# Optimization experiments

Hardware: AMD Instinct MI355X
Metric: run time of the kernel (lower is better)

## Reference

```python
import jax, jax.numpy as jnp
import numpy as np

B, D, C, M = 16384, 512, 1000, 8


def setup_inputs() -> dict:
    key = jax.random.key(0)
    k1, k2, k3, k4 = jax.random.split(key, 4)
    x = jax.random.normal(k1, (B, D), dtype=jnp.float32)
    W = jax.random.normal(k2, (M, D, C), dtype=jnp.float32) * 0.02
    b = jax.random.normal(k3, (M, C), dtype=jnp.float32) * 0.02
    coefs = jax.random.uniform(k4, (M,), dtype=jnp.float32, minval=0.5, maxval=1.5)
    return {"x": x, "W": W, "b": b, "coefs": coefs}


def reference(x, W, b, coefs):
    # Per-model logits: [M, B, C]
    logits = jnp.einsum('bd,mdc->mbc', x, W) + b[:, None, :]
    pos = jnp.argmax(logits, axis=-1)  # [M, B] predicted class per model/sample
    rows = jnp.broadcast_to(jnp.arange(x.shape[0])[None, :], pos.shape)  # [M, B]
    # Weighted vote scatter-add: ans[j, pos[m, j]] += coefs[m]
    ans = jnp.zeros((x.shape[0], W.shape[2]), dtype=jnp.float32)
    ans = ans.at[rows, pos].add(jnp.broadcast_to(coefs[:, None], pos.shape))
    return ans / W.shape[0]
```

## Files before the change

### kernel.cpp

```cpp
#include <hip/hip_runtime.h>

#define B_N 16384
#define D_K 512
#define C_N 1000
#define CP 1024
#define M_N 8
#define GAP_EPS 1e-3f

typedef __attribute__((ext_vector_type(8))) _Float16 f16x8;
typedef __attribute__((ext_vector_type(4))) float f32x4;

typedef const __attribute__((address_space(1))) unsigned int* gptr_t;
typedef __attribute__((address_space(3))) unsigned int* lptr_t;

__device__ __forceinline__ void gload16(const void* g, void* l) {
    __builtin_amdgcn_global_load_lds((gptr_t)g, (lptr_t)l, 16, 0, 0);
}

#define BAR()        asm volatile("s_barrier" ::: "memory")
#define WAIT_LGKM0() asm volatile("s_waitcnt lgkmcnt(0)" ::: "memory")
#define WAIT_VM6()   asm volatile("s_waitcnt vmcnt(6)" ::: "memory")
#define WAIT_VM0()   asm volatile("s_waitcnt vmcnt(0)" ::: "memory")

__device__ __forceinline__ unsigned short h16(float f) {
    _Float16 h = (_Float16)f;
    return *(unsigned short*)&h;
}


__global__ __launch_bounds__(256) void ve_conv(const float* __restrict__ x,
        const float* __restrict__ W, unsigned short* __restrict__ xf,
        unsigned short* __restrict__ wt, unsigned int* __restrict__ cnts) {
    const int tid = threadIdx.x;
    if (blockIdx.x < 8192) {
        int i = blockIdx.x * 256 + tid;
        if (blockIdx.x == 0 && tid < M_N) cnts[tid] = 0u;
        float4 v = reinterpret_cast<const float4*>(x)[i];
        ushort4 h;
        h.x = h16(v.x); h.y = h16(v.y); h.z = h16(v.z); h.w = h16(v.w);
        reinterpret_cast<ushort4*>(xf)[i] = h;
    } else {
        __shared__ float t[64][65];
        const int b = blockIdx.x - 8192;
        const int c0 = (b & 15) * 64, k0 = ((b >> 4) & 7) * 64, m = b >> 7;
#pragma unroll
        for (int p = 0; p < 16; ++p) {
            int idx = p * 256 + tid;
            int kk = idx >> 6, cc = idx & 63;
            int c = c0 + cc;
            t[kk][cc] = (c < C_N) ? W[((size_t)m * D_K + k0 + kk) * C_N + c] : 0.f;
        }
        __syncthreads();
#pragma unroll
        for (int p = 0; p < 4; ++p) {
            int idx = p * 256 + tid;
            int cc = idx >> 4, kq = idx & 15;
            ushort4 h;
            h.x = h16(t[kq * 4 + 0][cc]); h.y = h16(t[kq * 4 + 1][cc]);
            h.z = h16(t[kq * 4 + 2][cc]); h.w = h16(t[kq * 4 + 3][cc]);
            size_t o = ((size_t)m * CP + c0 + cc) * D_K + k0 + kq * 4;
            *reinterpret_cast<ushort4*>(wt + o) = h;
        }
    }
}


__global__ __launch_bounds__(256, 2) void ve_gemm16d(
        const unsigned short* __restrict__ Xf, const unsigned short* __restrict__ WT,
        const float* __restrict__ bias, float4* __restrict__ part) {
    __shared__ unsigned short At[12288];
    __shared__ unsigned short Bt[24576];

    const int tid = threadIdx.x;
    const int l = tid & 63, w = tid >> 6;
    const int wr = w >> 1, wc = w & 1;
    const int l15 = l & 15, kg = l >> 4;
    const int bid = blockIdx.x;
    const int mb = bid & 7, ct = (bid >> 3) & 3, rt = bid >> 5;
    const int r0 = rt * 128, c0 = ct * 256;

    const int lhi = l >> 3, llo = l & 7;
    const int s3g = llo ^ lhi;
    const int srow16 = (lhi << 1) | (s3g >> 2);
    const int kgs = (s3g & 3) * 8;

    const unsigned short* xA0 = Xf + (size_t)(r0 +      w * 16 + srow16) * D_K + kgs;
    const unsigned short* xA1 = Xf + (size_t)(r0 + 64 + w * 16 + srow16) * D_K + kgs;
    const unsigned short* xB0 = WT + (size_t)(mb * CP + c0 +       w * 16 + srow16) * D_K + kgs;
    const unsigned short* xB1 = WT + (size_t)(mb * CP + c0 +  64 + w * 16 + srow16) * D_K + kgs;
    const unsigned short* xB2 = WT + (size_t)(mb * CP + c0 + 128 + w * 16 + srow16) * D_K + kgs;
    const unsigned short* xB3 = WT + (size_t)(mb * CP + c0 + 192 + w * 16 + srow16) * D_K + kgs;

    auto stage = [&](int t, int buf) {
        unsigned short* A = At + buf * 4096;
        unsigned short* B = Bt + buf * 8192;
        gload16(xA0 + t * 32, A + tid * 8);
        gload16(xA1 + t * 32, A + 2048 + tid * 8);
        gload16(xB0 + t * 32, B + tid * 8);
        gload16(xB1 + t * 32, B + 2048 + tid * 8);
        gload16(xB2 + t * 32, B + 4096 + tid * 8);
        gload16(xB3 + t * 32, B + 6144 + tid * 8);
    };

    auto ldsoff = [&](int row, int kc) {
        return (row >> 1) * 64 + (((((row & 1) << 2) | kc) ^ ((row >> 1) & 7)) * 8);
    };
    const char* aP[4]; const char* bP[8];
#pragma unroll
    for (int i = 0; i < 4; ++i)
        aP[i] = (const char*)At + 2 * ldsoff(wr * 64 + i * 16 + l15, kg);
#pragma unroll
    for (int j = 0; j < 8; ++j)
        bP[j] = (const char*)Bt + wc * 8192 + 2 * ldsoff(j * 16 + l15, kg);

    f32x4 acc[4][8];
#pragma unroll
    for (int i = 0; i < 4; ++i)
#pragma unroll
        for (int j = 0; j < 8; ++j) acc[i][j] = (f32x4){0.f, 0.f, 0.f, 0.f};

    stage(0, 0);
    stage(1, 1);
    WAIT_VM6();
    BAR();

#pragma unroll 1
    for (int t = 0; t < 16; ++t) {
        if (t < 14) stage(t + 2, (t + 2) % 3);
        const int curA = (t % 3) * 8192;
        const int curB = (t % 3) * 16384;

        f16x8 af[4], bf[8];
#pragma unroll
        for (int i = 0; i < 4; ++i) af[i] = *reinterpret_cast<const f16x8*>(aP[i] + curA);
#pragma unroll
        for (int j = 0; j < 8; ++j) bf[j] = *reinterpret_cast<const f16x8*>(bP[j] + curB);
        __builtin_amdgcn_s_setprio(1);
#pragma unroll
        for (int i = 0; i < 4; ++i)
#pragma unroll
            for (int j = 0; j < 8; ++j)
                acc[i][j] = __builtin_amdgcn_mfma_f32_16x16x32_f16(af[i], bf[j], acc[i][j], 0, 0, 0);
        __builtin_amdgcn_s_setprio(0);

        if (t < 14)       { WAIT_VM6(); }
        else if (t == 14) { WAIT_VM0(); }
        WAIT_LGKM0();
        BAR();
    }

    float4 (*wtop)[2] = reinterpret_cast<float4(*)[2]>(At);

    float bv[8]; int cg[8];
#pragma unroll
    for (int j = 0; j < 8; ++j) {
        int c = c0 + wc * 128 + j * 16 + l15;
        cg[j] = c;
        bv[j] = (c < C_N) ? bias[mb * C_N + c] : -1e30f;
    }
#pragma unroll
    for (int i = 0; i < 4; ++i) {
#pragma unroll
        for (int reg = 0; reg < 4; ++reg) {
            float v1 = acc[i][0][reg] + bv[0]; int i1 = cg[0];
            float v2 = -1e30f;
#pragma unroll
            for (int j = 1; j < 8; ++j) {
                float v = acc[i][j][reg] + bv[j];
                float mn = fminf(v, v1);
                v2 = fmaxf(v2, mn);
                i1 = (v > v1) ? cg[j] : i1;
                v1 = fmaxf(v1, v);
            }
#pragma unroll
            for (int mask = 1; mask < 16; mask <<= 1) {
                float ov1 = __shfl_xor(v1, mask);
                int   oi1 = __shfl_xor(i1, mask);
                float ov2 = __shfl_xor(v2, mask);
                float mn = fminf(v1, ov1);
                v2 = fmaxf(fmaxf(v2, ov2), mn);
                i1 = (ov1 > v1) ? oi1 : i1;
                v1 = fmaxf(v1, ov1);
            }
            if (l15 == 0) {
                int row = wr * 64 + i * 16 + (l >> 4) * 4 + reg;
                wtop[row][wc] = make_float4(v1, __int_as_float(i1), v2, 0.f);
            }
        }
    }
    __syncthreads();
    if (tid < 128) {
        float4 a = wtop[tid][0], b = wtop[tid][1];
        float v1, v2; int i1;
        if (b.x > a.x) {
            v1 = b.x; i1 = __float_as_int(b.y);
            v2 = fmaxf(a.x, b.z);
        } else {
            v1 = a.x; i1 = __float_as_int(a.y);
            v2 = fmaxf(b.x, a.z);
        }
        part[((size_t)mb * B_N + r0 + tid) * 4 + ct] =
            make_float4(v1, __int_as_float(i1), v2, 0.f);
    }
}


__global__ __launch_bounds__(128) void ve_flag4(const float4* __restrict__ part,
        unsigned int* __restrict__ wout, unsigned int* __restrict__ rlist,
        unsigned int* __restrict__ cnts) {
    int r = blockIdx.x * 128 + threadIdx.x;
#pragma unroll
    for (int m = 0; m < M_N; ++m) {
        float4 o = part[((size_t)m * B_N + r) * 4 + 0];
        float v1 = o.x; int i1 = __float_as_int(o.y); float v2 = o.z;
#pragma unroll
        for (int t = 1; t < 4; ++t) {
            float4 q = part[((size_t)m * B_N + r) * 4 + t];
            if (q.x > v1) {
                v2 = fmaxf(v1, fmaxf(q.z, v2));
                v1 = q.x; i1 = __float_as_int(q.y);
            } else {
                v2 = fmaxf(v2, q.x);
            }
        }
        wout[m * B_N + r] = (unsigned)i1;
        if (v1 - v2 <= GAP_EPS) {
            unsigned pos = atomicAdd(&cnts[m], 1u);
            rlist[m * B_N + pos] = (unsigned)r;
        }
    }
}


__global__ __launch_bounds__(256) void ve_exact_g(
        const float* __restrict__ x, const float* __restrict__ W,
        const float* __restrict__ bias, const unsigned int* __restrict__ rlist,
        const unsigned int* __restrict__ cnts, float2* __restrict__ part2) {
    __shared__ float xs[32][65];
    __shared__ float wsm[32][128];
    __shared__ int rg[64];
    const int ct = blockIdx.x, m = blockIdx.z;
    const int tid = threadIdx.x;
    const int tx = tid & 15, ty = tid >> 4;
    const int c0 = ct * 128;
    const unsigned nm = cnts[m];

    for (unsigned rb = blockIdx.y; rb * 64 < nm; rb += gridDim.y) {
        __syncthreads();
        if (tid < 64) {
            unsigned idx = rb * 64 + tid;
            rg[tid] = (idx < nm) ? (int)rlist[m * B_N + idx] : 0;
        }
        __syncthreads();

        float acc[4][8];
#pragma unroll
        for (int i = 0; i < 4; i++)
#pragma unroll
            for (int j = 0; j < 8; j++) acc[i][j] = 0.f;

        for (int kt = 0; kt < D_K; kt += 32) {
#pragma unroll
            for (int i = 0; i < 2; i++) {
                int li = tid + i * 256;
                int row = li >> 3, kq = li & 7;
                float4 v = *reinterpret_cast<const float4*>(
                        x + (size_t)rg[row] * D_K + kt + kq * 4);
                int kk = kq * 4;
                xs[kk + 0][row] = v.x; xs[kk + 1][row] = v.y;
                xs[kk + 2][row] = v.z; xs[kk + 3][row] = v.w;
            }
#pragma unroll
            for (int i = 0; i < 4; i++) {
                int li = tid + i * 256;
                int kk = li >> 5, cq = li & 31;
                int c = c0 + cq * 4;
                const float* p = W + ((size_t)(m * D_K + kt + kk)) * C_N + c;
                float4 v;
                if (c + 3 < C_N) v = *reinterpret_cast<const float4*>(p);
                else {
                    v.x = (c + 0 < C_N) ? p[0] : 0.f; v.y = (c + 1 < C_N) ? p[1] : 0.f;
                    v.z = (c + 2 < C_N) ? p[2] : 0.f; v.w = (c + 3 < C_N) ? p[3] : 0.f;
                }
                wsm[kk][cq * 4 + 0] = v.x; wsm[kk][cq * 4 + 1] = v.y;
                wsm[kk][cq * 4 + 2] = v.z; wsm[kk][cq * 4 + 3] = v.w;
            }
            __syncthreads();
            for (int kk = 0; kk < 32; kk++) {
                float a[4], bb[8];
#pragma unroll
                for (int i = 0; i < 4; i++) a[i] = xs[kk][ty + i * 16];
#pragma unroll
                for (int j = 0; j < 8; j++) bb[j] = wsm[kk][tx + j * 16];
#pragma unroll
                for (int i = 0; i < 4; i++)
#pragma unroll
                    for (int j = 0; j < 8; j++) acc[i][j] += a[i] * bb[j];
            }
            __syncthreads();
        }

        const float NEG_INF = -__builtin_huge_valf();
        float bv[8]; int cv[8];
#pragma unroll
        for (int j = 0; j < 8; j++) {
            int c = c0 + tx + j * 16;
            cv[j] = c;
            bv[j] = (c < C_N) ? bias[m * C_N + c] : 0.f;
        }
#pragma unroll
        for (int i = 0; i < 4; i++) {
            float best = NEG_INF; int bidx = 0x7fffffff;
#pragma unroll
            for (int j = 0; j < 8; j++) {
                int c = cv[j];
                float v = (c < C_N) ? (acc[i][j] + bv[j]) : NEG_INF;
                if (v > best || (v == best && c < bidx)) { best = v; bidx = c; }
            }
#pragma unroll
            for (int mask = 1; mask < 16; mask <<= 1) {
                float ov = __shfl_xor(best, mask);
                int oi = __shfl_xor(bidx, mask);
                if (ov > best || (ov == best && oi < bidx)) { best = ov; bidx = oi; }
            }
            unsigned slot = rb * 64 + ty + i * 16;
            if (tx == 0 && slot < nm)
                part2[((size_t)m * B_N + slot) * 8 + ct] = make_float2(best, __int_as_float(bidx));
        }
    }
}

__global__ __launch_bounds__(256) void ve_merge_x(const float2* __restrict__ part2,
        const unsigned int* __restrict__ rlist, const unsigned int* __restrict__ cnts,
        unsigned int* __restrict__ wout) {
    int gid = blockIdx.x * 256 + threadIdx.x;
    int m = gid >> 14, s = gid & (B_N - 1);
    if (s < (int)cnts[m]) {
        const float NEG_INF = -__builtin_huge_valf();
        float best = NEG_INF; int bidx = 0x7fffffff;
#pragma unroll
        for (int ctt = 0; ctt < 8; ctt++) {
            float2 p = part2[((size_t)m * B_N + s) * 8 + ctt];
            int oi = __float_as_int(p.y);
            if (p.x > best || (p.x == best && oi < bidx)) { best = p.x; bidx = oi; }
        }
        wout[m * B_N + rlist[m * B_N + s]] = (unsigned)bidx;
    }
}

__global__ __launch_bounds__(256) void ve_votef(const unsigned int* __restrict__ wout,
        const float* __restrict__ coefs, float* __restrict__ out) {
    const int tid = threadIdx.x;
    const int r0 = blockIdx.x * 64;
    float4* po = reinterpret_cast<float4*>(out + (size_t)r0 * C_N);
    const float4 z = make_float4(0.f, 0.f, 0.f, 0.f);
    for (int i = tid; i < 16000; i += 256) po[i] = z;
    __syncthreads();
    if (tid < 64) {
        int r = r0 + tid;
#pragma unroll
        for (int m = 0; m < M_N; ++m)
            out[(size_t)r * C_N + wout[m * B_N + r]] += coefs[m] * 0.125f;
    }
}


#define TM 128
#define TN 128
#define TK 32
#define CT 8

__global__ __launch_bounds__(256) void ve_zero_out(float* __restrict__ out, int n4) {
    int i = blockIdx.x * blockDim.x + threadIdx.x;
    const float4 z = make_float4(0.f, 0.f, 0.f, 0.f);
    for (; i < n4; i += gridDim.x * blockDim.x)
        reinterpret_cast<float4*>(out)[i] = z;
}

__global__ __launch_bounds__(256) void ve_gemm_argmax_fb(
        const float* __restrict__ x, const float* __restrict__ W,
        const float* __restrict__ bias, float2* __restrict__ part) {
    __shared__ float xs[TK][TM + 1];
    __shared__ float ws[TK][TN];
    const int ct = blockIdx.x, rt = blockIdx.y, m = blockIdx.z;
    const int tid = threadIdx.x;
    const int tx = tid & 15, ty = tid >> 4;
    const int r0 = rt * TM, c0 = ct * TN;
    float acc[8][8];
#pragma unroll
    for (int i = 0; i < 8; i++)
#pragma unroll
        for (int j = 0; j < 8; j++) acc[i][j] = 0.f;
    const float* xbase = x + (size_t)r0 * D_K;
    for (int kt = 0; kt < D_K; kt += TK) {
#pragma unroll
        for (int i = 0; i < 4; i++) {
            int li = tid + i * 256;
            int row = li >> 3, kq = li & 7;
            float4 v = *reinterpret_cast<const float4*>(xbase + (size_t)row * D_K + kt + kq * 4);
            int kk = kq * 4;
            xs[kk + 0][row] = v.x; xs[kk + 1][row] = v.y;
            xs[kk + 2][row] = v.z; xs[kk + 3][row] = v.w;
        }
#pragma unroll
        for (int i = 0; i < 4; i++) {
            int li = tid + i * 256;
            int kk = li >> 5, cq = li & 31;
            int c = c0 + cq * 4;
            const float* p = W + ((size_t)(m * D_K + kt + kk)) * C_N + c;
            float4 v;
            if (c + 3 < C_N) v = *reinterpret_cast<const float4*>(p);
            else {
                v.x = (c + 0 < C_N) ? p[0] : 0.f; v.y = (c + 1 < C_N) ? p[1] : 0.f;
                v.z = (c + 2 < C_N) ? p[2] : 0.f; v.w = (c + 3 < C_N) ? p[3] : 0.f;
            }
            ws[kk][cq * 4 + 0] = v.x; ws[kk][cq * 4 + 1] = v.y;
            ws[kk][cq * 4 + 2] = v.z; ws[kk][cq * 4 + 3] = v.w;
        }
        __syncthreads();
        for (int kk = 0; kk < TK; kk++) {
            float a[8], bb[8];
#pragma unroll
            for (int i = 0; i < 8; i++) a[i] = xs[kk][ty + i * 16];
#pragma unroll
            for (int j = 0; j < 8; j++) bb[j] = ws[kk][tx + j * 16];
#pragma unroll
            for (int i = 0; i < 8; i++)
#pragma unroll
                for (int j = 0; j < 8; j++) acc[i][j] += a[i] * bb[j];
        }
        __syncthreads();
    }
    const float NEG_INF = -__builtin_huge_valf();
    float bv[8]; int cv[8];
#pragma unroll
    for (int j = 0; j < 8; j++) {
        int c = c0 + tx + j * 16;
        cv[j] = c;
        bv[j] = (c < C_N) ? bias[m * C_N + c] : 0.f;
    }
#pragma unroll
    for (int i = 0; i < 8; i++) {
        int r = r0 + ty + i * 16;
        float best = NEG_INF; int bidx = 0x7fffffff;
#pragma unroll
        for (int j = 0; j < 8; j++) {
            int c = cv[j];
            float v = (c < C_N) ? (acc[i][j] + bv[j]) : NEG_INF;
            if (v > best || (v == best && c < bidx)) { best = v; bidx = c; }
        }
#pragma unroll
        for (int mask = 1; mask < 16; mask <<= 1) {
            float ov = __shfl_xor(best, mask);
            int oi = __shfl_xor(bidx, mask);
            if (ov > best || (ov == best && oi < bidx)) { best = ov; bidx = oi; }
        }
        if (tx == 0) part[((size_t)m * B_N + r) * CT + ct] = make_float2(best, __int_as_float(bidx));
    }
}

__global__ __launch_bounds__(256) void ve_vote_fb(const float2* __restrict__ part,
        const float* __restrict__ coefs, float* __restrict__ out) {
    int r = blockIdx.x * blockDim.x + threadIdx.x;
    if (r >= B_N) return;
    const float NEG_INF = -__builtin_huge_valf();
#pragma unroll
    for (int m = 0; m < M_N; m++) {
        float best = NEG_INF; int bidx = 0x7fffffff;
#pragma unroll
        for (int ctt = 0; ctt < CT; ctt++) {
            float2 p = part[((size_t)m * B_N + r) * CT + ctt];
            int oi = __float_as_int(p.y);
            if (p.x > best || (p.x == best && oi < bidx)) { best = p.x; bidx = oi; }
        }
        out[(size_t)r * C_N + bidx] += coefs[m] * 0.125f;
    }
}


extern "C" void kernel_launch(void* const* d_in, const int* in_sizes, int n_in,
                              void* d_out, int out_size, void* d_ws, size_t ws_size,
                              hipStream_t stream) {
    const float* x     = (const float*)d_in[0];
    const float* W     = (const float*)d_in[1];
    const float* bias  = (const float*)d_in[2];
    const float* coefs = (const float*)d_in[3];
    float* out = (float*)d_out;

    const size_t NEED = (57ull << 20) + 4096;
    if (ws_size >= NEED) {
        char* ws = (char*)d_ws;
        unsigned short* Xf    = (unsigned short*)(ws);
        unsigned short* WT16  = (unsigned short*)(ws + (16ull << 20));
        float4*         part  = (float4*)(ws + (24ull << 20));
        float2*         part2 = (float2*)(ws + (40ull << 20));
        unsigned int*   wout  = (unsigned int*)(ws + (48ull << 20));
        unsigned int*   rlist = (unsigned int*)(ws + (48ull << 20) + (512ull << 10));
        unsigned int*   cnts  = (unsigned int*)(ws + (49ull << 20));

        ve_conv<<<9216, 256, 0, stream>>>(x, W, Xf, WT16, cnts);
        ve_gemm16d<<<4096, 256, 0, stream>>>(Xf, WT16, bias, part);
        ve_flag4<<<128, 128, 0, stream>>>(part, wout, rlist, cnts);
        ve_exact_g<<<dim3(8, 8, 8), 256, 0, stream>>>(x, W, bias, rlist, cnts, part2);
        ve_merge_x<<<512, 256, 0, stream>>>(part2, rlist, cnts, wout);
        ve_votef<<<256, 256, 0, stream>>>(wout, coefs, out);
    } else {
        float2* partf = (float2*)d_ws;
        ve_zero_out<<<2048, 256, 0, stream>>>(out, B_N * C_N / 4);
        dim3 grid(CT, B_N / TM, M_N);
        ve_gemm_argmax_fb<<<grid, 256, 0, stream>>>(x, W, bias, partf);
        ve_vote_fb<<<(B_N + 255) / 256, 256, 0, stream>>>(partf, coefs, out);
    }
}
```

Baseline: 314.9 us.

## Merge exact-fix results via 64-bit atomicMax and fold output zeroing into conversion

Removes the ve_merge_x kernel: ve_exact_g now writes each column-tile's best (value, index) into a per-row 64-bit key with atomicMax. The key packs an order-preserving float key with the inverted index, so ties still go to the smaller index. ve_flag4 marks ambiguous rows with a high bit in wout, and ve_votef reads the fixed key only for those rows. Zeroing the output moves into extra blocks of the conversion kernel, so votef no longer clears out before scattering. This drops one launch and the part2 buffer traffic, at the cost of global atomics and extra conversion blocks.

```diff
diff --git a/kernel.cpp b/kernel.cpp
--- a/kernel.cpp
+++ b/kernel.cpp
@@ -27,10 +27,16 @@
     return *(unsigned short*)&h;
 }
 
+__device__ __forceinline__ unsigned fkey32(float f) {
+    unsigned u = __float_as_uint(f);
+    return (u & 0x80000000u) ? ~u : (u | 0x80000000u);
+}
+
 
 __global__ __launch_bounds__(256) void ve_conv(const float* __restrict__ x,
         const float* __restrict__ W, unsigned short* __restrict__ xf,
-        unsigned short* __restrict__ wt, unsigned int* __restrict__ cnts) {
+        unsigned short* __restrict__ wt, unsigned int* __restrict__ cnts,
+        float* __restrict__ out) {
     const int tid = threadIdx.x;
     if (blockIdx.x < 8192) {
         int i = blockIdx.x * 256 + tid;
@@ -39,7 +45,7 @@
         ushort4 h;
         h.x = h16(v.x); h.y = h16(v.y); h.z = h16(v.z); h.w = h16(v.w);
         reinterpret_cast<ushort4*>(xf)[i] = h;
-    } else {
+    } else if (blockIdx.x < 9216) {
         __shared__ float t[64][65];
         const int b = blockIdx.x - 8192;
         const int c0 = (b & 15) * 64, k0 = ((b >> 4) & 7) * 64, m = b >> 7;
@@ -61,6 +67,11 @@
             size_t o = ((size_t)m * CP + c0 + cc) * D_K + k0 + kq * 4;
             *reinterpret_cast<ushort4*>(wt + o) = h;
         }
+    } else {
+        const int b = blockIdx.x - 9216;
+        float4* po = reinterpret_cast<float4*>(out) + (size_t)b * 4000;
+        const float4 z = make_float4(0.f, 0.f, 0.f, 0.f);
+        for (int i = tid; i < 4000; i += 256) po[i] = z;
     }
 }
 
@@ -207,7 +218,7 @@
 
 __global__ __launch_bounds__(128) void ve_flag4(const float4* __restrict__ part,
         unsigned int* __restrict__ wout, unsigned int* __restrict__ rlist,
-        unsigned int* __restrict__ cnts) {
+        unsigned int* __restrict__ cnts, unsigned long long* __restrict__ fixkey) {
     int r = blockIdx.x * 128 + threadIdx.x;
 #pragma unroll
     for (int m = 0; m < M_N; ++m) {
@@ -223,10 +234,13 @@
                 v2 = fmaxf(v2, q.x);
             }
         }
-        wout[m * B_N + r] = (unsigned)i1;
         if (v1 - v2 <= GAP_EPS) {
+            wout[m * B_N + r] = (unsigned)i1 | 0x80000000u;
+            fixkey[m * B_N + r] = 0ull;
             unsigned pos = atomicAdd(&cnts[m], 1u);
             rlist[m * B_N + pos] = (unsigned)r;
+        } else {
+            wout[m * B_N + r] = (unsigned)i1;
         }
     }
 }
@@ -235,7 +249,7 @@
 __global__ __launch_bounds__(256) void ve_exact_g(
         const float* __restrict__ x, const float* __restrict__ W,
         const float* __restrict__ bias, const unsigned int* __restrict__ rlist,
-        const unsigned int* __restrict__ cnts, float2* __restrict__ part2) {
+        const unsigned int* __restrict__ cnts, unsigned long long* __restrict__ fixkey) {
     __shared__ float xs[32][65];
     __shared__ float wsm[32][128];
     __shared__ int rg[64];
@@ -324,43 +338,30 @@
                 if (ov > best || (ov == best && oi < bidx)) { best = ov; bidx = oi; }
             }
             unsigned slot = rb * 64 + ty + i * 16;
-            if (tx == 0 && slot < nm)
-                part2[((size_t)m * B_N + slot) * 8 + ct] = make_float2(best, __int_as_float(bidx));
-        }
-    }
-}
-
-__global__ __launch_bounds__(256) void ve_merge_x(const float2* __restrict__ part2,
-        const unsigned int* __restrict__ rlist, const unsigned int* __restrict__ cnts,
-        unsigned int* __restrict__ wout) {
-    int gid = blockIdx.x * 256 + threadIdx.x;
-    int m = gid >> 14, s = gid & (B_N - 1);
-    if (s < (int)cnts[m]) {
-        const float NEG_INF = -__builtin_huge_valf();
-        float best = NEG_INF; int bidx = 0x7fffffff;
-#pragma unroll
-        for (int ctt = 0; ctt < 8; ctt++) {
-            float2 p = part2[((size_t)m * B_N + s) * 8 + ctt];
-            int oi = __float_as_int(p.y);
-            if (p.x > best || (p.x == best && oi < bidx)) { best = p.x; bidx = oi; }
-        }
-        wout[m * B_N + rlist[m * B_N + s]] = (unsigned)bidx;
-    }
-}
-
-__global__ __launch_bounds__(256) void ve_votef(const unsigned int* __restrict__ wout,
+            if (tx == 0 && slot < nm) {
+                unsigned long long key =
+                    ((unsigned long long)fkey32(best) << 32) | (unsigned)(~(unsigned)bidx);
+                atomicMax(fixkey + (size_t)m * B_N + rg[ty + i * 16], key);
+            }
+        }
+    }
+}
+
+__global__ __launch_bounds__(128) void ve_votef(const unsigned int* __restrict__ wout,
+        const unsigned long long* __restrict__ fixkey,
         const float* __restrict__ coefs, float* __restrict__ out) {
-    const int tid = threadIdx.x;
-    const int r0 = blockIdx.x * 64;
-    float4* po = reinterpret_cast<float4*>(out + (size_t)r0 * C_N);
-    const float4 z = make_float4(0.f, 0.f, 0.f, 0.f);
-    for (int i = tid; i < 16000; i += 256) po[i] = z;
-    __syncthreads();
-    if (tid < 64) {
-        int r = r0 + tid;
-#pragma unroll
-        for (int m = 0; m < M_N; ++m)
-            out[(size_t)r * C_N + wout[m * B_N + r]] += coefs[m] * 0.125f;
+    int r = blockIdx.x * 128 + threadIdx.x;
+#pragma unroll
+    for (int m = 0; m < M_N; ++m) {
+        unsigned wv = wout[m * B_N + r];
+        int idx;
+        if (wv & 0x80000000u) {
+            unsigned long long k = fixkey[(size_t)m * B_N + r];
+            idx = (int)(~(unsigned)k);
+        } else {
+            idx = (int)wv;
+        }
+        out[(size_t)r * C_N + idx] += coefs[m] * 0.125f;
     }
 }
 
@@ -490,20 +491,19 @@
     const size_t NEED = (57ull << 20) + 4096;
     if (ws_size >= NEED) {
         char* ws = (char*)d_ws;
-        unsigned short* Xf    = (unsigned short*)(ws);
-        unsigned short* WT16  = (unsigned short*)(ws + (16ull << 20));
-        float4*         part  = (float4*)(ws + (24ull << 20));
-        float2*         part2 = (float2*)(ws + (40ull << 20));
-        unsigned int*   wout  = (unsigned int*)(ws + (48ull << 20));
-        unsigned int*   rlist = (unsigned int*)(ws + (48ull << 20) + (512ull << 10));
-        unsigned int*   cnts  = (unsigned int*)(ws + (49ull << 20));
-
-        ve_conv<<<9216, 256, 0, stream>>>(x, W, Xf, WT16, cnts);
+        unsigned short*     Xf     = (unsigned short*)(ws);
+        unsigned short*     WT16   = (unsigned short*)(ws + (16ull << 20));
+        float4*             part   = (float4*)(ws + (24ull << 20));
+        unsigned long long* fixkey = (unsigned long long*)(ws + (40ull << 20));
+        unsigned int*       wout   = (unsigned int*)(ws + (48ull << 20));
+        unsigned int*       rlist  = (unsigned int*)(ws + (48ull << 20) + (512ull << 10));
+        unsigned int*       cnts   = (unsigned int*)(ws + (49ull << 20));
+
+        ve_conv<<<10240, 256, 0, stream>>>(x, W, Xf, WT16, cnts, out);
         ve_gemm16d<<<4096, 256, 0, stream>>>(Xf, WT16, bias, part);
-        ve_flag4<<<128, 128, 0, stream>>>(part, wout, rlist, cnts);
-        ve_exact_g<<<dim3(8, 8, 8), 256, 0, stream>>>(x, W, bias, rlist, cnts, part2);
-        ve_merge_x<<<512, 256, 0, stream>>>(part2, rlist, cnts, wout);
-        ve_votef<<<256, 256, 0, stream>>>(wout, coefs, out);
+        ve_flag4<<<128, 128, 0, stream>>>(part, wout, rlist, cnts, fixkey);
+        ve_exact_g<<<dim3(8, 8, 8), 256, 0, stream>>>(x, W, bias, rlist, cnts, fixkey);
+        ve_votef<<<128, 128, 0, stream>>>(wout, fixkey, coefs, out);
     } else {
         float2* partf = (float2*)d_ws;
         ve_zero_out<<<2048, 256, 0, stream>>>(out, B_N * C_N / 4);
```

Result: no change. 311.2 us (median of 2 runs) (-1.2%).
